# Kernel tuning notes

Measured on AMD Instinct MI355X. Metric: run time of the kernel, lower is better.

## Reference

```python
import jax, jax.numpy as jnp
import numpy as np

H, W = 256, 512
SCORE_THR = 0.2
NMS_THR = 0.15
TOPK = 4096


def _make_anchors():
    xs = (np.arange(W) + 0.5) * 0.4 - 0.2 * W
    ys = (np.arange(H) + 0.5) * 0.4 - 0.2 * H
    gx, gy = np.meshgrid(xs, ys)            # [H, W]
    anc = np.zeros((H, W, 2, 7), dtype=np.float32)
    anc[..., 0] = gx[..., None]
    anc[..., 1] = gy[..., None]
    anc[..., 2] = -1.0
    anc[..., 3] = 1.56  # h
    anc[..., 4] = 1.6   # w
    anc[..., 5] = 3.9   # l
    anc[..., 0, 6] = 0.0
    anc[..., 1, 6] = np.pi / 2
    return jnp.asarray(anc)


def _make_T(theta, tx, ty, tz):
    c, s = np.cos(theta), np.sin(theta)
    T = np.eye(4, dtype=np.float32)
    T[0, 0], T[0, 1], T[1, 0], T[1, 1] = c, -s, s, c
    T[0, 3], T[1, 3], T[2, 3] = tx, ty, tz
    return jnp.asarray(T)


def setup_inputs() -> dict:
    key = jax.random.key(0)
    k1, k2, k3, k4 = jax.random.split(key, 4)
    return {
        "anchors": _make_anchors(),
        "psm_v": jax.random.normal(k1, (1, 2, H, W), jnp.float32),
        "rm_v": jax.random.normal(k2, (1, 14, H, W), jnp.float32) * 0.1,
        "psm_i": jax.random.normal(k3, (1, 2, H, W), jnp.float32),
        "rm_i": jax.random.normal(k4, (1, 14, H, W), jnp.float32) * 0.1,
        "t_proj": _make_T(0.05, 2.0, -1.0, 0.1),
        "t_ego": _make_T(-0.1, 5.0, 3.0, 0.0),
    }


def delta_to_boxes3d(rm, anchors):
    # rm: [1, 14, H, W] -> [A, 7]; anchors: [H, W, 2, 7] xyzhwlr -> [A, 7]
    d = jnp.transpose(rm[0], (1, 2, 0)).reshape(-1, 7)
    a = anchors.reshape(-1, 7)
    ad = jnp.sqrt(a[:, 4] ** 2 + a[:, 5] ** 2)          # diag of w,l
    xy = d[:, :2] * ad[:, None] + a[:, :2]
    z = d[:, 2] * a[:, 3] + a[:, 2]
    dims = jnp.exp(d[:, 3:6]) * a[:, 3:6]               # h, w, l
    yaw = d[:, 6] + a[:, 6]
    return jnp.concatenate([xy, z[:, None], dims, yaw[:, None]], axis=1)


def boxes_to_corners_3d(b):
    # b: [N, 7] x,y,z,h,w,l,yaw (order 'hwl') -> [N, 8, 3]
    h, w, l, yaw = b[:, 3], b[:, 4], b[:, 5], b[:, 6]
    sx = jnp.array([1, 1, -1, -1, 1, 1, -1, -1], jnp.float32) * 0.5
    sy = jnp.array([1, -1, -1, 1, 1, -1, -1, 1], jnp.float32) * 0.5
    sz = jnp.array([-1, -1, -1, -1, 1, 1, 1, 1], jnp.float32) * 0.5
    x = l[:, None] * sx
    y = w[:, None] * sy
    z = h[:, None] * sz
    c, s = jnp.cos(yaw)[:, None], jnp.sin(yaw)[:, None]
    xr = x * c - y * s + b[:, 0:1]
    yr = x * s + y * c + b[:, 1:2]
    zr = z + b[:, 2:3]
    return jnp.stack([xr, yr, zr], axis=-1)


def project_box3d(corners, T):
    # corners: [N, 8, 3]; T: [4, 4]
    return jnp.einsum('ij,nkj->nki', T[:3, :3], corners) + T[:3, 3]


def corner_to_center(corners):
    # inverse of boxes_to_corners_3d, order 'hwl'
    xyz = corners.mean(axis=1)
    h = corners[:, 4:, 2].mean(axis=1) - corners[:, :4, 2].mean(axis=1)
    dl = corners[:, (0, 1, 4, 5), :2] - corners[:, (3, 2, 7, 6), :2]
    dw = corners[:, (0, 3, 4, 7), :2] - corners[:, (1, 2, 5, 6), :2]
    l = jnp.linalg.norm(dl, axis=-1).mean(axis=1)
    w = jnp.linalg.norm(dw, axis=-1).mean(axis=1)
    d = dl.sum(axis=1)
    yaw = jnp.arctan2(d[:, 1], d[:, 0])
    return jnp.concatenate(
        [xyz, h[:, None], w[:, None], l[:, None], yaw[:, None]], axis=1)


def standup_boxes(corners):
    # [N, 8, 3] -> [N, 4] x1,y1,x2,y2 over BEV
    mn = corners[..., :2].min(axis=1)
    mx = corners[..., :2].max(axis=1)
    return jnp.concatenate([mn, mx], axis=1)


def iou_matrix(b):
    area = (b[:, 2] - b[:, 0]) * (b[:, 3] - b[:, 1])
    lt = jnp.maximum(b[:, None, :2], b[None, :, :2])
    rb = jnp.minimum(b[:, None, 2:], b[None, :, 2:])
    wh = jnp.clip(rb - lt, 0.0)
    inter = wh[..., 0] * wh[..., 1]
    return inter / (area[:, None] + area[None, :] - inter + 1e-6)


def nms_keep(iou, valid, thresh):
    K = iou.shape[0]
    idx = jnp.arange(K)

    def body(i, keep):
        sup = (iou[i] > thresh) & (idx > i) & keep[i]
        return keep & ~sup

    return jax.lax.fori_loop(0, K, body, valid)


def _branch(psm, rm, anchors):
    scores = jax.nn.sigmoid(jnp.transpose(psm[0], (1, 2, 0))).reshape(-1)
    boxes = delta_to_boxes3d(rm, anchors)
    return boxes, scores


def reference(anchors, psm_v, rm_v, psm_i, rm_i, t_proj, t_ego):
    boxes_v, scores_v = _branch(psm_v, rm_v, anchors)
    boxes_i, scores_i = _branch(psm_i, rm_i, anchors)
    # project infra branch boxes into ego frame via corner transform
    corners_i = boxes_to_corners_3d(boxes_i)
    boxes_i = corner_to_center(project_box3d(corners_i, t_proj))
    boxes = jnp.concatenate([boxes_v, boxes_i], axis=0)       # [2A, 7]
    scores = jnp.concatenate([scores_v, scores_i], axis=0)    # [2A]
    # project all to ego space
    proj = project_box3d(boxes_to_corners_3d(boxes), t_ego)   # [2A, 8, 3]
    # static replacement of masked_select: mask + top-K
    masked = jnp.where(scores > SCORE_THR, scores, -1.0)
    top_s, top_i = jax.lax.top_k(masked, TOPK)
    corners_k = proj[top_i]                                    # [K, 8, 3]
    iou = iou_matrix(standup_boxes(corners_k))
    keep = nms_keep(iou, top_s > SCORE_THR, NMS_THR)
    final = top_s * keep.astype(top_s.dtype)
    # pack corners + surviving scores: [K, 25]
    return jnp.concatenate([corners_k.reshape(TOPK, 24), final[:, None]], axis=1)
```

## Files before the change

kernel.cpp:

```cpp
#include <hip/hip_runtime.h>
#include <stdint.h>

typedef unsigned int u32;
typedef unsigned long long u64;

#define HH 256
#define WW 512
#define HW (HH*WW)
#define N2 (2*HW)
#define NT (2*N2)
#define TOPK 4096
#define SCORE_THR 0.2f
#define NMS_THR 0.15f

#define OFF_KEYS   0ull
#define OFF_GHIST  ((size_t)NT*4)
#define OFF_GHIST2 (OFF_GHIST + 4096)
#define OFF_CNT    (OFF_GHIST2 + 4096)
#define OFF_VALIDM (OFF_CNT + 16)
#define OFF_CAND   (OFF_VALIDM + 512)
#define OFF_STAND  OFF_CAND
#define OFF_SELIDX (OFF_CAND + 65536)
#define OFF_SELSC  (OFF_SELIDX + (size_t)TOPK*4)
#define OFF_TDIAG  (OFF_SELSC + (size_t)TOPK*4)
#define ZERO_BYTES (4096 + 4096 + 16)
#define RANK_J 8

#define NMSW 4
#define RPW 16
#define WREG_U64 1088
#define SLOT_U64 (NMSW * WREG_U64)

__device__ __forceinline__ u32 f2ord(float f) {
    u32 b = __float_as_uint(f);
    return (b & 0x80000000u) ? ~b : (b | 0x80000000u);
}

__global__ void __launch_bounds__(1024) k_keys(const float* __restrict__ psm_v,
                                               const float* __restrict__ psm_i,
                                               u32* __restrict__ keys,
                                               u32* __restrict__ ghist) {
    __shared__ u32 lh[1024];
    int t = threadIdx.x;
    lh[t] = 0;
    __syncthreads();
    int n = blockIdx.x * 1024 + t;
    int br = n >> 18;
    int m  = n & (N2 - 1);
    int a  = m & 1;
    int hw = m >> 1;
    const float* psm = br ? psm_i : psm_v;
    float x = psm[a * HW + hw];
    float s = 1.0f / (1.0f + __builtin_expf(-x));
    u32 key = 0u;
    if (s > SCORE_THR) key = f2ord(s);
    keys[n] = key;
    if (key) atomicAdd(&lh[key >> 22], 1u);
    __syncthreads();
    u32 c = lh[t];
    if (c) atomicAdd(&ghist[t], c);
}

__device__ __forceinline__ void pivot1024(const u32* __restrict__ arr, u32 target,
                                          u32* out_bin, u32* out_next, int l) {
    u32 h[16], loc[16];
#pragma unroll
    for (int j = 0; j < 16; ++j) h[j] = arr[l * 16 + j];
    loc[15] = h[15];
#pragma unroll
    for (int j = 14; j >= 0; --j) loc[j] = loc[j + 1] + h[j];
    u32 T = loc[0];
    u32 incl = T;
#pragma unroll
    for (int d = 1; d < 64; d <<= 1) {
        u32 v = __shfl_down(incl, d);
        if (l + d < 64) incl += v;
    }
    u32 E = incl - T;
#pragma unroll
    for (int j = 0; j < 16; ++j) {
        u32 S  = loc[j] + E;
        u32 Sn = (j < 15 ? loc[j + 1] : 0u) + E;
        if (S >= target && Sn < target) {
            *out_bin = (u32)(l * 16 + j);
            *out_next = Sn;
        }
    }
}

__global__ void __launch_bounds__(1024) k_hist2(const u32* __restrict__ ghist,
                                                const u32* __restrict__ keys,
                                                u32* __restrict__ ghist2) {
    __shared__ u32 lh[1024];
    __shared__ u32 b1_sh;
    int tid = threadIdx.x;
    lh[tid] = 0;
    if (tid < 64) {
        u32 bin = 0xFFFFFFFFu, nxt = 0;
        pivot1024(ghist, (u32)TOPK, &bin, &nxt, tid);
        if (bin != 0xFFFFFFFFu) b1_sh = bin;
    }
    __syncthreads();
    u32 b1 = b1_sh;
    int n = blockIdx.x * 1024 + tid;
    u32 key = keys[n];
    if ((key >> 22) == b1) atomicAdd(&lh[(key >> 12) & 1023u], 1u);
    __syncthreads();
    u32 c = lh[tid];
    if (c) atomicAdd(&ghist2[tid], c);
}

__global__ void __launch_bounds__(1024) k_collect(const u32* __restrict__ ghist,
                                                  const u32* __restrict__ ghist2,
                                                  const u32* __restrict__ keys,
                                                  u64* __restrict__ cand,
                                                  u32* __restrict__ cnt) {
    __shared__ u32 b1_sh, t2_sh, b2_sh;
    int tid = threadIdx.x;
    if (tid < 64) {
        u32 bin = 0xFFFFFFFFu, nxt = 0;
        pivot1024(ghist, (u32)TOPK, &bin, &nxt, tid);
        if (bin != 0xFFFFFFFFu) { b1_sh = bin; t2_sh = (u32)TOPK - nxt; }
    }
    __syncthreads();
    if (tid < 64) {
        u32 bin = 0xFFFFFFFFu, nxt = 0;
        pivot1024(ghist2, t2_sh, &bin, &nxt, tid);
        if (bin != 0xFFFFFFFFu) b2_sh = bin;
    }
    __syncthreads();
    u32 thr20 = (b1_sh << 10) | b2_sh;
    int n = blockIdx.x * 1024 + tid;
    u32 key = keys[n];
    if ((key >> 12) >= thr20) {
        u32 pos = atomicAdd(cnt, 1u);
        if (pos < 8192u)
            cand[pos] = ((u64)key << 32) | (u64)(u32)(~(u32)n);
    }
}

__global__ void __launch_bounds__(256) k_rank1(const u64* __restrict__ cand,
                                               const u32* __restrict__ cnt,
                                               u32* __restrict__ partial,
                                               u32* __restrict__ done,
                                               u32* __restrict__ sel_idx) {
    __shared__ u64 tile[1024];
    __shared__ u32 lastsh;
    int tid = threadIdx.x;
    int i = blockIdx.x * 256 + tid;
    u32 base = blockIdx.y * 1024u;
    u32 c = *cnt;
    if (c > 8192u) c = 8192u;
    u64 my = (i < (int)c) ? cand[i] : 0ull;
#pragma unroll
    for (int k = 0; k < 4; ++k) {
        u32 idx = base + tid + k * 256;
        tile[tid + k * 256] = (idx < c) ? cand[idx] : 0ull;
    }
    __syncthreads();
    u32 lim = (c > base) ? ((c - base < 1024u) ? (c - base) : 1024u) : 0u;
    u32 r = 0;
#pragma unroll 4
    for (u32 k = 0; k < lim; ++k) r += (tile[k] > my) ? 1u : 0u;
    partial[blockIdx.y * 8192 + i] = r;
    __threadfence();
    __syncthreads();
    if (tid == 0)
        lastsh = (atomicAdd(done, 1u) == (u32)(32 * RANK_J - 1)) ? 1u : 0u;
    __syncthreads();
    if (lastsh) {
        __threadfence();
        for (u32 it = tid; it < c; it += 256u) {
            u32 rank = 0;
#pragma unroll
            for (int bj = 0; bj < RANK_J; ++bj) rank += partial[bj * 8192 + it];
            if (rank < (u32)TOPK)
                sel_idx[rank] = ~((u32)(cand[it] & 0xFFFFFFFFull));
        }
    }
}

__device__ __forceinline__ void box_corners(const float b[7], float cx[8], float cy[8], float cz[8]) {
    const float sx[8] = {0.5f,0.5f,-0.5f,-0.5f,0.5f,0.5f,-0.5f,-0.5f};
    const float sy[8] = {0.5f,-0.5f,-0.5f,0.5f,0.5f,-0.5f,-0.5f,0.5f};
    const float sz[8] = {-0.5f,-0.5f,-0.5f,-0.5f,0.5f,0.5f,0.5f,0.5f};
    float c = __builtin_cosf(b[6]), s = __builtin_sinf(b[6]);
#pragma unroll
    for (int k = 0; k < 8; k++) {
        float x = b[5] * sx[k], y = b[4] * sy[k], z = b[3] * sz[k];
        cx[k] = x * c - y * s + b[0];
        cy[k] = x * s + y * c + b[1];
        cz[k] = z + b[2];
    }
}

__device__ __forceinline__ void proj_T(const float* __restrict__ T, float cx[8], float cy[8], float cz[8]) {
#pragma unroll
    for (int k = 0; k < 8; k++) {
        float x = cx[k], y = cy[k], z = cz[k];
        cx[k] = T[0] * x + T[1] * y + T[2]  * z + T[3];
        cy[k] = T[4] * x + T[5] * y + T[6]  * z + T[7];
        cz[k] = T[8] * x + T[9] * y + T[10] * z + T[11];
    }
}

__device__ __forceinline__ void corner_to_center(const float cx[8], const float cy[8], const float cz[8], float b[7]) {
    float mx = 0.f, my = 0.f, mz = 0.f;
#pragma unroll
    for (int k = 0; k < 8; k++) { mx += cx[k]; my += cy[k]; mz += cz[k]; }
    mx *= 0.125f; my *= 0.125f; mz *= 0.125f;
    float htop = (cz[4] + cz[5] + cz[6] + cz[7]) * 0.25f;
    float hbot = (cz[0] + cz[1] + cz[2] + cz[3]) * 0.25f;
    const int lA[4] = {0,1,4,5}, lB[4] = {3,2,7,6};
    const int wA[4] = {0,3,4,7}, wB[4] = {1,2,5,6};
    float l = 0.f, w = 0.f, dx = 0.f, dy = 0.f;
#pragma unroll
    for (int i = 0; i < 4; i++) {
        float ax = cx[lA[i]] - cx[lB[i]];
        float ay = cy[lA[i]] - cy[lB[i]];
        l += __builtin_sqrtf(ax * ax + ay * ay);
        dx += ax; dy += ay;
    }
#pragma unroll
    for (int i = 0; i < 4; i++) {
        float ax = cx[wA[i]] - cx[wB[i]];
        float ay = cy[wA[i]] - cy[wB[i]];
        w += __builtin_sqrtf(ax * ax + ay * ay);
    }
    b[0] = mx; b[1] = my; b[2] = mz;
    b[3] = htop - hbot;
    b[4] = w * 0.25f;
    b[5] = l * 0.25f;
    b[6] = atan2f(dy, dx);
}

__global__ void __launch_bounds__(64) k_boxes(const float* __restrict__ anchors,
                                              const float* __restrict__ psm_v,
                                              const float* __restrict__ psm_i,
                                              const float* __restrict__ rm_v,
                                              const float* __restrict__ rm_i,
                                              const float* __restrict__ tproj,
                                              const float* __restrict__ tego,
                                              const u32* __restrict__ sel_idx,
                                              float* __restrict__ sel_sc,
                                              float* __restrict__ out,
                                              float4* __restrict__ stand,
                                              u64* __restrict__ validm) {
    int k = blockIdx.x * blockDim.x + threadIdx.x;
    if (k >= TOPK) return;
    int n = (int)(sel_idx[k] & (u32)(NT - 1));
    int br = n >> 18;
    int m  = n & (N2 - 1);
    int a  = m & 1;
    int hw = m >> 1;

    const float* psm = br ? psm_i : psm_v;
    float xs = psm[a * HW + hw];
    float s  = 1.0f / (1.0f + __builtin_expf(-xs));
    sel_sc[k] = (s > SCORE_THR) ? s : -1.0f;
    u64 vbits = __ballot(s > SCORE_THR);
    if ((threadIdx.x & 63) == 0) validm[k >> 6] = vbits;

    const float* rm = br ? rm_i : rm_v;
    float d[7];
#pragma unroll
    for (int j = 0; j < 7; j++) d[j] = rm[(a * 7 + j) * HW + hw];
    const float* anc = anchors + (size_t)m * 7;
    float a0 = anc[0], a1 = anc[1], a2 = anc[2], a3 = anc[3], a4 = anc[4], a5 = anc[5], a6 = anc[6];
    float ad = __builtin_sqrtf(a4 * a4 + a5 * a5);
    float b[7];
    b[0] = d[0] * ad + a0;
    b[1] = d[1] * ad + a1;
    b[2] = d[2] * a3 + a2;
    b[3] = __builtin_expf(d[3]) * a3;
    b[4] = __builtin_expf(d[4]) * a4;
    b[5] = __builtin_expf(d[5]) * a5;
    b[6] = d[6] + a6;

    if (br) {
        float cx[8], cy[8], cz[8];
        box_corners(b, cx, cy, cz);
        proj_T(tproj, cx, cy, cz);
        corner_to_center(cx, cy, cz, b);
    }

    float cx[8], cy[8], cz[8];
    box_corners(b, cx, cy, cz);
    proj_T(tego, cx, cy, cz);

    float mnx = cx[0], mny = cy[0], mxx = cx[0], mxy = cy[0];
#pragma unroll
    for (int c = 0; c < 8; c++) {
        out[(size_t)k * 25 + c * 3 + 0] = cx[c];
        out[(size_t)k * 25 + c * 3 + 1] = cy[c];
        out[(size_t)k * 25 + c * 3 + 2] = cz[c];
        mnx = fminf(mnx, cx[c]); mny = fminf(mny, cy[c]);
        mxx = fmaxf(mxx, cx[c]); mxy = fmaxf(mxy, cy[c]);
    }
    stand[k] = make_float4(mnx, mny, mxx, mxy);
}

__global__ void __launch_bounds__(256) k_maskdiag(const float4* __restrict__ stand,
                                                  u64* __restrict__ mask,
                                                  u64* __restrict__ tdiag) {
    __shared__ float4 sb[256];
    int bid = blockIdx.x;
    if (bid < 1024) {
        int i = bid * 4 + (threadIdx.x >> 6);
        int t = threadIdx.x & 63;
        int w0 = i >> 6;
        float4 bi = stand[i];
        float areai = (bi.z - bi.x) * (bi.w - bi.y);
        u64 myword = 0ull;
        for (int w = w0; w < 64; ++w) {
            int j = w * 64 + t;
            float4 bj = stand[j];
            float areaj = (bj.z - bj.x) * (bj.w - bj.y);
            float ltx = fmaxf(bi.x, bj.x), lty = fmaxf(bi.y, bj.y);
            float rbx = fminf(bi.z, bj.z), rby = fminf(bi.w, bj.w);
            float iw = fmaxf(rbx - ltx, 0.0f), ih = fmaxf(rby - lty, 0.0f);
            float inter = iw * ih;
            float iou = inter / (areai + areaj - inter + 1e-6f);
            bool sup = (iou > NMS_THR) && (j > i);
            u64 bits = __ballot(sup);
            if (t == w) myword = bits;
        }
        mask[(size_t)i * 64 + t] = myword;
    } else {
        int d = bid - 1024;
        int tid = threadIdx.x;
        sb[tid] = stand[d * 256 + tid];
        __syncthreads();
        int sub = tid >> 6, l = tid & 63;
        float4 me = sb[sub * 64 + l];
        float aream = (me.z - me.x) * (me.w - me.y);
        u64 T = 0ull;
        for (int j = 0; j < 64; ++j) {
            float4 bj = sb[sub * 64 + j];
            float areaj = (bj.z - bj.x) * (bj.w - bj.y);
            float ltx = fmaxf(bj.x, me.x), lty = fmaxf(bj.y, me.y);
            float rbx = fminf(bj.z, me.z), rby = fminf(bj.w, me.w);
            float iw = fmaxf(rbx - ltx, 0.0f), ih = fmaxf(rby - lty, 0.0f);
            float inter = iw * ih;
            float iou = inter / (areaj + aream - inter + 1e-6f);
            bool sup = (iou > NMS_THR) && (j < l);
            T |= sup ? (1ull << j) : 0ull;
        }
        tdiag[(size_t)(d * 4 + sub) * 64 + l] = T;
    }
}

__device__ __forceinline__ u64 readlane64(u64 v, int lane) {
    u32 lo = (u32)__builtin_amdgcn_readlane((int)(u32)v, lane);
    u32 hi = (u32)__builtin_amdgcn_readlane((int)(u32)(v >> 32), lane);
    return ((u64)hi << 32) | (u64)lo;
}

__device__ __forceinline__ void nms_stage(const u64* __restrict__ mask,
                                          const u64* __restrict__ tdiag,
                                          int c, int sw, int l, u64* wb) {
    bool act = (2 * (l & 31) + 1) >= c;
    const u64* gb = mask + (size_t)c * 4096 + (size_t)(sw * RPW) * 64 + (size_t)l * 2;
    if (act) {
#pragma unroll
        for (int k = 0; k < 8; ++k) {
            __builtin_amdgcn_global_load_lds(
                (const __attribute__((address_space(1))) void*)(gb + (size_t)k * 128),
                (__attribute__((address_space(3))) void*)(wb + (size_t)k * 128), 16, 0, 0);
        }
    }
    if (l < 32) {
        __builtin_amdgcn_global_load_lds(
            (const __attribute__((address_space(1))) void*)(tdiag + (size_t)c * 64 + (size_t)l * 2),
            (__attribute__((address_space(3))) void*)(wb + 1024), 16, 0, 0);
    }
}

__device__ __forceinline__ void nms_ldrows(const u64* wb, int l,
                                           u64 (&rows)[RPW], u64& Tl) {
    Tl = wb[1024 + l];
#pragma unroll
    for (int k = 0; k < RPW; ++k) rows[k] = wb[(size_t)k * 64 + l];
}

template<int VMC, bool REFILL, bool PRELOAD>
__device__ __forceinline__ void nms_chunk(int B, int l, int sw,
                                          const u64 (&rows)[RPW], u64 Tl,
                                          u64 (&nrows)[RPW], u64& nTl,
                                          u64* wb_cur, u64* wb_next,
                                          u64 vreg, volatile u64* sh,
                                          u64& remv, u64& keep,
                                          const u64* __restrict__ mask,
                                          const u64* __restrict__ tdiag) {
    u64 x = readlane64(remv, B);
    if (l == 0) sh[(B & 1) * NMSW + sw] = x;
    __asm__ volatile("" ::: "memory");
    __builtin_amdgcn_s_waitcnt(0xC07F);
    __builtin_amdgcn_s_barrier();
    __asm__ volatile("" ::: "memory");
    if constexpr (VMC == 9) __builtin_amdgcn_s_waitcnt(0x0F79);
    else if constexpr (VMC == 0) __builtin_amdgcn_s_waitcnt(0x0F70);
    __builtin_amdgcn_sched_barrier(0);
    __asm__ volatile("" ::: "memory");
    if constexpr (REFILL) nms_stage(mask, tdiag, B + 3, sw, l, wb_cur);
    if constexpr (PRELOAD) nms_ldrows(wb_next, l, nrows, nTl);
    __builtin_amdgcn_sched_barrier(0);
    const volatile u64* sp = sh + (B & 1) * NMSW;
    u64 curw = sp[0] | sp[1] | sp[2] | sp[3];
    u64 vm = readlane64(vreg, B);
    u64 ve = vm & ~curw;
    u64 D = 0ull, P = ve;
    while (D != P) {
        u64 nD = ve & ~__ballot((Tl & P) != 0ull);
        u64 nP = ve & ~__ballot((Tl & nD) != 0ull);
        D = nD; P = nP;
    }
    u64 kb = D;
    keep = (l == B) ? kb : keep;
    u64 kbw = (kb >> (sw * RPW)) & 0xFFFFull;
    u64 p = 0ull;
#pragma unroll
    for (int k = 0; k < RPW; ++k)
        p |= rows[k] & (0ull - ((kbw >> k) & 1ull));
    remv |= p;
}

__global__ void __launch_bounds__(NMSW * 64, 1)
k_nms(const u64* __restrict__ mask,
      const u64* __restrict__ tdiag,
      const u64* __restrict__ validm,
      const float* __restrict__ sc,
      float* __restrict__ out) {
    __shared__ u64 ring[3 * SLOT_U64];
    __shared__ u64 sh[2 * NMSW];
    int l  = threadIdx.x & 63;
    int sw = __builtin_amdgcn_readfirstlane((int)(threadIdx.x >> 6));
    u64 remv = 0ull;
    u64 keep = 0ull;
    u64 vreg = validm[l];

    u64* wbs0 = ring + 0 * SLOT_U64 + (size_t)sw * WREG_U64;
    u64* wbs1 = ring + 1 * SLOT_U64 + (size_t)sw * WREG_U64;
    u64* wbs2 = ring + 2 * SLOT_U64 + (size_t)sw * WREG_U64;
    nms_stage(mask, tdiag, 0, sw, l, wbs0);
    nms_stage(mask, tdiag, 1, sw, l, wbs1);
    nms_stage(mask, tdiag, 2, sw, l, wbs2);
    __builtin_amdgcn_s_waitcnt(0x4F72);
    __builtin_amdgcn_sched_barrier(0);
    __asm__ volatile("" ::: "memory");
    u64 rowA[RPW], rowB[RPW], TlA, TlB;
    nms_ldrows(wbs0, l, rowA, TlA);

    int sA = 0;
    for (int B = 0; B < 60; B += 2) {
        int s1 = sA + 1; if (s1 == 3) s1 = 0;
        int s2 = s1 + 1; if (s2 == 3) s2 = 0;
        u64* wbA = ring + (size_t)sA * SLOT_U64 + (size_t)sw * WREG_U64;
        u64* wbB = ring + (size_t)s1 * SLOT_U64 + (size_t)sw * WREG_U64;
        u64* wbC = ring + (size_t)s2 * SLOT_U64 + (size_t)sw * WREG_U64;
        nms_chunk<9, true, true>(B,     l, sw, rowA, TlA, rowB, TlB, wbA, wbB,
                                 vreg, sh, remv, keep, mask, tdiag);
        nms_chunk<9, true, true>(B + 1, l, sw, rowB, TlB, rowA, TlA, wbB, wbC,
                                 vreg, sh, remv, keep, mask, tdiag);
        sA = s2;
    }
    {
        int s1 = sA + 1; if (s1 == 3) s1 = 0;
        int s2 = s1 + 1; if (s2 == 3) s2 = 0;
        u64* wb60 = ring + (size_t)sA * SLOT_U64 + (size_t)sw * WREG_U64;
        u64* wb61 = ring + (size_t)s1 * SLOT_U64 + (size_t)sw * WREG_U64;
        u64* wb62 = ring + (size_t)s2 * SLOT_U64 + (size_t)sw * WREG_U64;
        u64* wb63 = wb60;
        nms_chunk<9,  true,  true >(60, l, sw, rowA, TlA, rowB, TlB, wb60, wb61,
                                    vreg, sh, remv, keep, mask, tdiag);
        nms_chunk<9,  false, true >(61, l, sw, rowB, TlB, rowA, TlA, wb61, wb62,
                                    vreg, sh, remv, keep, mask, tdiag);
        nms_chunk<0,  false, true >(62, l, sw, rowA, TlA, rowB, TlB, wb62, wb63,
                                    vreg, sh, remv, keep, mask, tdiag);
        nms_chunk<-1, false, false>(63, l, sw, rowB, TlB, rowA, TlA, wb63, wb63,
                                    vreg, sh, remv, keep, mask, tdiag);
    }

    for (int k = 0; k < RPW; ++k) {
        int c = sw * RPW + k;
        u64 kc = readlane64(keep, c);
        float s = sc[c * 64 + l];
        out[(size_t)(c * 64 + l) * 25 + 24] = ((kc >> l) & 1ull) ? s : 0.0f;
    }
}

extern "C" void kernel_launch(void* const* d_in, const int* in_sizes, int n_in,
                              void* d_out, int out_size, void* d_ws, size_t ws_size,
                              hipStream_t stream) {
    const float* anchors = (const float*)d_in[0];
    const float* psm_v   = (const float*)d_in[1];
    const float* rm_v    = (const float*)d_in[2];
    const float* psm_i   = (const float*)d_in[3];
    const float* rm_i    = (const float*)d_in[4];
    const float* tproj   = (const float*)d_in[5];
    const float* tego    = (const float*)d_in[6];
    float* out = (float*)d_out;
    char* ws = (char*)d_ws;

    u32*    keys    = (u32*)(ws + OFF_KEYS);
    u64*    mask    = (u64*)(ws + OFF_KEYS);
    u32*    partial = (u32*)(ws + OFF_KEYS);
    u32*    ghist   = (u32*)(ws + OFF_GHIST);
    u32*    ghist2  = (u32*)(ws + OFF_GHIST2);
    u32*    cnt     = (u32*)(ws + OFF_CNT);
    u32*    done    = (u32*)(ws + OFF_CNT + 4);
    u64*    validm  = (u64*)(ws + OFF_VALIDM);
    u64*    cand    = (u64*)(ws + OFF_CAND);
    float4* stand   = (float4*)(ws + OFF_STAND);
    u32*    sel_idx = (u32*)(ws + OFF_SELIDX);
    float*  sel_sc  = (float*)(ws + OFF_SELSC);
    u64*    tdiag   = (u64*)(ws + OFF_TDIAG);

    hipMemsetAsync(ws + OFF_GHIST, 0, ZERO_BYTES, stream);
    k_keys    <<<NT / 1024, 1024, 0, stream>>>(psm_v, psm_i, keys, ghist);
    k_hist2   <<<NT / 1024, 1024, 0, stream>>>(ghist, keys, ghist2);
    k_collect <<<NT / 1024, 1024, 0, stream>>>(ghist, ghist2, keys, cand, cnt);
    k_rank1   <<<dim3(32, RANK_J), 256, 0, stream>>>(cand, cnt, partial, done, sel_idx);
    k_boxes   <<<TOPK / 64, 64, 0, stream>>>(anchors, psm_v, psm_i, rm_v, rm_i,
                                             tproj, tego, sel_idx, sel_sc, out,
                                             stand, validm);
    k_maskdiag<<<1040, 256, 0, stream>>>(stand, mask, tdiag);
    k_nms     <<<1, NMSW * 64, 0, stream>>>(mask, tdiag, validm, sel_sc, out);
}
```

Baseline: 269.1 us.

## Split rank scatter and mask/diag into separate kernels, hoist NMS shared reads

Removes the last-block atomic counter and threadfence pattern from the rank kernel by adding a separate scatter kernel. Splits the combined mask/diagonal kernel into two kernels, raises the box kernel block size to 256, and moves the shared-memory reads of the suppression words ahead of the waitcnt/sched barrier in the NMS chunk. The aim is to cut serialized single-block tail work and latency on the NMS critical path. The cost is two extra kernel launches and their launch overhead.

Result: faster. 235.7 us (-12.4%).

```diff
diff --git a/kernel.cpp b/kernel.cpp
--- a/kernel.cpp
+++ b/kernel.cpp
@@ -141,11 +141,8 @@
 
 __global__ void __launch_bounds__(256) k_rank1(const u64* __restrict__ cand,
                                                const u32* __restrict__ cnt,
-                                               u32* __restrict__ partial,
-                                               u32* __restrict__ done,
-                                               u32* __restrict__ sel_idx) {
+                                               u32* __restrict__ partial) {
     __shared__ u64 tile[1024];
-    __shared__ u32 lastsh;
     int tid = threadIdx.x;
     int i = blockIdx.x * 256 + tid;
     u32 base = blockIdx.y * 1024u;
@@ -163,20 +160,22 @@
 #pragma unroll 4
     for (u32 k = 0; k < lim; ++k) r += (tile[k] > my) ? 1u : 0u;
     partial[blockIdx.y * 8192 + i] = r;
-    __threadfence();
-    __syncthreads();
-    if (tid == 0)
-        lastsh = (atomicAdd(done, 1u) == (u32)(32 * RANK_J - 1)) ? 1u : 0u;
-    __syncthreads();
-    if (lastsh) {
-        __threadfence();
-        for (u32 it = tid; it < c; it += 256u) {
-            u32 rank = 0;
-#pragma unroll
-            for (int bj = 0; bj < RANK_J; ++bj) rank += partial[bj * 8192 + it];
-            if (rank < (u32)TOPK)
-                sel_idx[rank] = ~((u32)(cand[it] & 0xFFFFFFFFull));
-        }
+}
+
+__global__ void __launch_bounds__(256) k_scatter(const u64* __restrict__ cand,
+                                                 const u32* __restrict__ cnt,
+                                                 const u32* __restrict__ partial,
+                                                 u32* __restrict__ sel_idx) {
+    int i = blockIdx.x * 256 + threadIdx.x;
+    u32 c = *cnt;
+    if (c > 8192u) c = 8192u;
+    if (i >= (int)c) return;
+    u32 rank = 0;
+#pragma unroll
+    for (int bj = 0; bj < RANK_J; ++bj) rank += partial[bj * 8192 + i];
+    if (rank < (u32)TOPK) {
+        u64 my = cand[i];
+        sel_idx[rank] = ~((u32)(my & 0xFFFFFFFFull));
     }
 }
 
@@ -234,18 +233,18 @@
     b[6] = atan2f(dy, dx);
 }
 
-__global__ void __launch_bounds__(64) k_boxes(const float* __restrict__ anchors,
-                                              const float* __restrict__ psm_v,
-                                              const float* __restrict__ psm_i,
-                                              const float* __restrict__ rm_v,
-                                              const float* __restrict__ rm_i,
-                                              const float* __restrict__ tproj,
-                                              const float* __restrict__ tego,
-                                              const u32* __restrict__ sel_idx,
-                                              float* __restrict__ sel_sc,
-                                              float* __restrict__ out,
-                                              float4* __restrict__ stand,
-                                              u64* __restrict__ validm) {
+__global__ void __launch_bounds__(256) k_boxes(const float* __restrict__ anchors,
+                                               const float* __restrict__ psm_v,
+                                               const float* __restrict__ psm_i,
+                                               const float* __restrict__ rm_v,
+                                               const float* __restrict__ rm_i,
+                                               const float* __restrict__ tproj,
+                                               const float* __restrict__ tego,
+                                               const u32* __restrict__ sel_idx,
+                                               float* __restrict__ sel_sc,
+                                               float* __restrict__ out,
+                                               float4* __restrict__ stand,
+                                               u64* __restrict__ validm) {
     int k = blockIdx.x * blockDim.x + threadIdx.x;
     if (k >= TOPK) return;
     int n = (int)(sel_idx[k] & (u32)(NT - 1));
@@ -300,54 +299,51 @@
     stand[k] = make_float4(mnx, mny, mxx, mxy);
 }
 
-__global__ void __launch_bounds__(256) k_maskdiag(const float4* __restrict__ stand,
-                                                  u64* __restrict__ mask,
-                                                  u64* __restrict__ tdiag) {
-    __shared__ float4 sb[256];
-    int bid = blockIdx.x;
-    if (bid < 1024) {
-        int i = bid * 4 + (threadIdx.x >> 6);
-        int t = threadIdx.x & 63;
-        int w0 = i >> 6;
-        float4 bi = stand[i];
-        float areai = (bi.z - bi.x) * (bi.w - bi.y);
-        u64 myword = 0ull;
-        for (int w = w0; w < 64; ++w) {
-            int j = w * 64 + t;
-            float4 bj = stand[j];
-            float areaj = (bj.z - bj.x) * (bj.w - bj.y);
-            float ltx = fmaxf(bi.x, bj.x), lty = fmaxf(bi.y, bj.y);
-            float rbx = fminf(bi.z, bj.z), rby = fminf(bi.w, bj.w);
-            float iw = fmaxf(rbx - ltx, 0.0f), ih = fmaxf(rby - lty, 0.0f);
-            float inter = iw * ih;
-            float iou = inter / (areai + areaj - inter + 1e-6f);
-            bool sup = (iou > NMS_THR) && (j > i);
-            u64 bits = __ballot(sup);
-            if (t == w) myword = bits;
-        }
-        mask[(size_t)i * 64 + t] = myword;
-    } else {
-        int d = bid - 1024;
-        int tid = threadIdx.x;
-        sb[tid] = stand[d * 256 + tid];
-        __syncthreads();
-        int sub = tid >> 6, l = tid & 63;
-        float4 me = sb[sub * 64 + l];
-        float aream = (me.z - me.x) * (me.w - me.y);
-        u64 T = 0ull;
-        for (int j = 0; j < 64; ++j) {
-            float4 bj = sb[sub * 64 + j];
-            float areaj = (bj.z - bj.x) * (bj.w - bj.y);
-            float ltx = fmaxf(bj.x, me.x), lty = fmaxf(bj.y, me.y);
-            float rbx = fminf(bj.z, me.z), rby = fminf(bj.w, me.w);
-            float iw = fmaxf(rbx - ltx, 0.0f), ih = fmaxf(rby - lty, 0.0f);
-            float inter = iw * ih;
-            float iou = inter / (areaj + aream - inter + 1e-6f);
-            bool sup = (iou > NMS_THR) && (j < l);
-            T |= sup ? (1ull << j) : 0ull;
-        }
-        tdiag[(size_t)(d * 4 + sub) * 64 + l] = T;
-    }
+__global__ void __launch_bounds__(256) k_mask(const float4* __restrict__ stand,
+                                              u64* __restrict__ mask) {
+    int i = blockIdx.x * 4 + (threadIdx.x >> 6);
+    int t = threadIdx.x & 63;
+    int w0 = i >> 6;
+    float4 bi = stand[i];
+    float areai = (bi.z - bi.x) * (bi.w - bi.y);
+    u64 myword = 0ull;
+    for (int w = w0; w < 64; ++w) {
+        int j = w * 64 + t;
+        float4 bj = stand[j];
+        float areaj = (bj.z - bj.x) * (bj.w - bj.y);
+        float ltx = fmaxf(bi.x, bj.x), lty = fmaxf(bi.y, bj.y);
+        float rbx = fminf(bi.z, bj.z), rby = fminf(bi.w, bj.w);
+        float iw = fmaxf(rbx - ltx, 0.0f), ih = fmaxf(rby - lty, 0.0f);
+        float inter = iw * ih;
+        float iou = inter / (areai + areaj - inter + 1e-6f);
+        bool sup = (iou > NMS_THR) && (j > i);
+        u64 bits = __ballot(sup);
+        if (t == w) myword = bits;
+    }
+    mask[(size_t)i * 64 + t] = myword;
+}
+
+__global__ void __launch_bounds__(64) k_diag(const float4* __restrict__ stand,
+                                             u64* __restrict__ tdiag) {
+    __shared__ float4 sb[64];
+    int B = blockIdx.x, l = threadIdx.x;
+    float4 me = stand[B * 64 + l];
+    sb[l] = me;
+    __syncthreads();
+    float aream = (me.z - me.x) * (me.w - me.y);
+    u64 T = 0ull;
+    for (int j = 0; j < 64; ++j) {
+        float4 bj = sb[j];
+        float areaj = (bj.z - bj.x) * (bj.w - bj.y);
+        float ltx = fmaxf(bj.x, me.x), lty = fmaxf(bj.y, me.y);
+        float rbx = fminf(bj.z, me.z), rby = fminf(bj.w, me.w);
+        float iw = fmaxf(rbx - ltx, 0.0f), ih = fmaxf(rby - lty, 0.0f);
+        float inter = iw * ih;
+        float iou = inter / (areaj + aream - inter + 1e-6f);
+        bool sup = (iou > NMS_THR) && (j < l);
+        T |= sup ? (1ull << j) : 0ull;
+    }
+    tdiag[B * 64 + l] = T;
 }
 
 __device__ __forceinline__ u64 readlane64(u64 v, int lane) {
@@ -398,15 +394,15 @@
     __builtin_amdgcn_s_waitcnt(0xC07F);
     __builtin_amdgcn_s_barrier();
     __asm__ volatile("" ::: "memory");
+    const volatile u64* sp = sh + (B & 1) * NMSW;
+    u64 c0 = sp[0], c1 = sp[1], c2 = sp[2], c3 = sp[3];
     if constexpr (VMC == 9) __builtin_amdgcn_s_waitcnt(0x0F79);
     else if constexpr (VMC == 0) __builtin_amdgcn_s_waitcnt(0x0F70);
     __builtin_amdgcn_sched_barrier(0);
-    __asm__ volatile("" ::: "memory");
     if constexpr (REFILL) nms_stage(mask, tdiag, B + 3, sw, l, wb_cur);
     if constexpr (PRELOAD) nms_ldrows(wb_next, l, nrows, nTl);
     __builtin_amdgcn_sched_barrier(0);
-    const volatile u64* sp = sh + (B & 1) * NMSW;
-    u64 curw = sp[0] | sp[1] | sp[2] | sp[3];
+    u64 curw = c0 | c1 | c2 | c3;
     u64 vm = readlane64(vreg, B);
     u64 ve = vm & ~curw;
     u64 D = 0ull, P = ve;
@@ -508,7 +504,6 @@
     u32*    ghist   = (u32*)(ws + OFF_GHIST);
     u32*    ghist2  = (u32*)(ws + OFF_GHIST2);
     u32*    cnt     = (u32*)(ws + OFF_CNT);
-    u32*    done    = (u32*)(ws + OFF_CNT + 4);
     u64*    validm  = (u64*)(ws + OFF_VALIDM);
     u64*    cand    = (u64*)(ws + OFF_CAND);
     float4* stand   = (float4*)(ws + OFF_STAND);
@@ -517,13 +512,15 @@
     u64*    tdiag   = (u64*)(ws + OFF_TDIAG);
 
     hipMemsetAsync(ws + OFF_GHIST, 0, ZERO_BYTES, stream);
-    k_keys    <<<NT / 1024, 1024, 0, stream>>>(psm_v, psm_i, keys, ghist);
-    k_hist2   <<<NT / 1024, 1024, 0, stream>>>(ghist, keys, ghist2);
-    k_collect <<<NT / 1024, 1024, 0, stream>>>(ghist, ghist2, keys, cand, cnt);
-    k_rank1   <<<dim3(32, RANK_J), 256, 0, stream>>>(cand, cnt, partial, done, sel_idx);
-    k_boxes   <<<TOPK / 64, 64, 0, stream>>>(anchors, psm_v, psm_i, rm_v, rm_i,
-                                             tproj, tego, sel_idx, sel_sc, out,
-                                             stand, validm);
-    k_maskdiag<<<1040, 256, 0, stream>>>(stand, mask, tdiag);
-    k_nms     <<<1, NMSW * 64, 0, stream>>>(mask, tdiag, validm, sel_sc, out);
-}
+    k_keys   <<<NT / 1024, 1024, 0, stream>>>(psm_v, psm_i, keys, ghist);
+    k_hist2  <<<NT / 1024, 1024, 0, stream>>>(ghist, keys, ghist2);
+    k_collect<<<NT / 1024, 1024, 0, stream>>>(ghist, ghist2, keys, cand, cnt);
+    k_rank1  <<<dim3(32, RANK_J), 256, 0, stream>>>(cand, cnt, partial);
+    k_scatter<<<32, 256, 0, stream>>>(cand, cnt, partial, sel_idx);
+    k_boxes  <<<TOPK / 256, 256, 0, stream>>>(anchors, psm_v, psm_i, rm_v, rm_i,
+                                              tproj, tego, sel_idx, sel_sc, out,
+                                              stand, validm);
+    k_mask   <<<TOPK / 4, 256, 0, stream>>>(stand, mask);
+    k_diag   <<<64, 64, 0, stream>>>(stand, tdiag);
+    k_nms    <<<1, NMSW * 64, 0, stream>>>(mask, tdiag, validm, sel_sc, out);
+}
```
